# Kernel tuning notes

Measured on AMD Instinct MI355X. Metric: run time of the kernel, lower is better.

Reference implementation:

```python
import jax, jax.numpy as jnp
import numpy as np

N_NODES = 50000
N_EDGES = 800000
D_IN = 128
D_HID = 200
D_OUT = 64
EPS = 0.0  # initial_eps, train_eps=False


def setup_inputs() -> dict:
    key = jax.random.key(0)
    ks = jax.random.split(key, 8)
    x = jax.random.normal(ks[0], (N_NODES, D_IN), dtype=jnp.float32)
    edge_row = jax.random.randint(ks[1], (N_EDGES,), 0, N_NODES)
    edge_col = jax.random.randint(ks[2], (N_EDGES,), 0, N_NODES)
    edge_val = jax.random.uniform(ks[3], (N_EDGES,), dtype=jnp.float32)
    W1 = jax.random.normal(ks[4], (D_IN, D_HID), dtype=jnp.float32) * 0.05
    b1 = jnp.zeros((D_HID,), dtype=jnp.float32)
    W2 = jax.random.normal(ks[5], (D_HID, D_OUT), dtype=jnp.float32) * 0.05
    b2 = jnp.zeros((D_OUT,), dtype=jnp.float32)
    return {"x": x, "edge_row": edge_row, "edge_col": edge_col,
            "edge_val": edge_val, "W1": W1, "b1": b1, "W2": W2, "b2": b2}


def reference(x, edge_row, edge_col, edge_val, W1, b1, W2, b2):
    # SpMM: agg[i] = sum_e val[e] * x[col[e]] for edges with row[e] == i
    msgs = edge_val[:, None] * x[edge_col]            # [E, D_IN] gather
    agg = jax.ops.segment_sum(msgs, edge_row, num_segments=N_NODES)  # [N, D_IN]
    # (1 + eps) * x + A @ x, then 2-layer MLP (Linear -> ReLU -> Linear)
    h = (1.0 + EPS) * x + agg
    h = jax.nn.relu(h @ W1 + b1)                      # [N, D_HID]
    out = h @ W2 + b2                                 # [N, D_OUT]
    return out
```

## Files before the change

### kernel.cpp

```cpp
#include <hip/hip_runtime.h>

#define NN 50000
#define NE 800000
#define DIN 128
#define DH 200
#define DHP 256
#define DO 64
#define RPB 32
#define NBUCK 1564
#define CAP 1024
#define EPB 8192
#define NBLK_E ((NE + EPB - 1) / EPB)
#define CVT_B 1563
#define PACK_B 12
#define NBIN 256

typedef float f32x4 __attribute__((ext_vector_type(4)));
typedef short bf16x8 __attribute__((ext_vector_type(8)));
typedef short s16x4 __attribute__((ext_vector_type(4)));
typedef unsigned int uint;

__device__ __forceinline__ unsigned short f2bf(float f) {
  unsigned int b = __float_as_uint(f);
  b = (b + 0x7FFFu + ((b >> 16) & 1u)) >> 16;
  return (unsigned short)b;
}
__device__ __forceinline__ float bf2f(unsigned short u) {
  return __uint_as_float((unsigned int)u << 16);
}

__global__ __launch_bounds__(512) void k_prep(const float* __restrict__ x,
                                              uint* __restrict__ xb,
                                              const int* __restrict__ row,
                                              int* __restrict__ hist,
                                              const float* __restrict__ W1,
                                              const float* __restrict__ W2,
                                              unsigned short* __restrict__ B1p,
                                              unsigned short* __restrict__ B2p) {
  __shared__ int lh[NBUCK];
  const int bid = blockIdx.x;
  const int tid = threadIdx.x;
  if (bid < CVT_B) {
    int i = bid * 512 + tid;
    if (i < NE) {
      f32x4 a = *reinterpret_cast<const f32x4*>(x + (size_t)i * 8);
      f32x4 b = *reinterpret_cast<const f32x4*>(x + (size_t)i * 8 + 4);
      uint4 o;
      o.x = (uint)f2bf(a[0]) | ((uint)f2bf(a[1]) << 16);
      o.y = (uint)f2bf(a[2]) | ((uint)f2bf(a[3]) << 16);
      o.z = (uint)f2bf(b[0]) | ((uint)f2bf(b[1]) << 16);
      o.w = (uint)f2bf(b[2]) | ((uint)f2bf(b[3]) << 16);
      *reinterpret_cast<uint4*>(xb + (size_t)i * 4) = o;
    }
  } else if (bid < CVT_B + NBLK_E) {
    const int hb = bid - CVT_B;
    const int e0 = hb * EPB;
    for (int j = tid; j < NBUCK; j += 512) lh[j] = 0;
    __syncthreads();
#pragma unroll
    for (int p = 0; p < EPB / 512; ++p) {
      int e = e0 + p * 512 + tid;
      if (e < NE) atomicAdd(&lh[row[e] >> 5], 1);
    }
    __syncthreads();
    int* hrow = hist + (size_t)hb * NBUCK;
    for (int j = tid; j < NBUCK; j += 512) hrow[j] = lh[j];
  } else {
    int gidx = (bid - CVT_B - NBLK_E) * 512 + tid;
    if (gidx < 4096) {
      int idx = gidx;
      int lane = idx & 63;
      int s = (idx >> 6) & 3;
      int t = idx >> 8;
      int n = t * 16 + (lane & 15);
      unsigned short v[8];
#pragma unroll
      for (int j = 0; j < 8; ++j) {
        int k = s * 32 + (j & 3) + ((lane >> 4) << 2) + ((j >> 2) << 4);
        float f = (n < DH) ? W1[(size_t)k * DH + n] : 0.f;
        v[j] = f2bf(f);
      }
      *reinterpret_cast<uint4*>(B1p + (size_t)idx * 8) =
          *reinterpret_cast<const uint4*>(v);
    } else if (gidx < 6144) {
      int idx = gidx - 4096;
      int lane = idx & 63;
      int s = (idx >> 6) & 7;
      int t = idx >> 9;
      int n = t * 16 + (lane & 15);
      unsigned short v[8];
#pragma unroll
      for (int j = 0; j < 8; ++j) {
        int k = s * 32 + (j & 3) + ((lane >> 4) << 2) + ((j >> 2) << 4);
        float f = (k < DH) ? W2[(size_t)k * DO + n] : 0.f;
        v[j] = f2bf(f);
      }
      *reinterpret_cast<uint4*>(B2p + (size_t)idx * 8) =
          *reinterpret_cast<const uint4*>(v);
    }
  }
}

__global__ __launch_bounds__(256) void k_scan(int* __restrict__ hist,
                                              int* __restrict__ cnt) {
  int k = blockIdx.x * 256 + threadIdx.x;
  if (k >= NBUCK) return;
  int run = 0;
  int b = 0;
  for (; b + 8 <= NBLK_E; b += 8) {
    int v0 = hist[(size_t)(b + 0) * NBUCK + k];
    int v1 = hist[(size_t)(b + 1) * NBUCK + k];
    int v2 = hist[(size_t)(b + 2) * NBUCK + k];
    int v3 = hist[(size_t)(b + 3) * NBUCK + k];
    int v4 = hist[(size_t)(b + 4) * NBUCK + k];
    int v5 = hist[(size_t)(b + 5) * NBUCK + k];
    int v6 = hist[(size_t)(b + 6) * NBUCK + k];
    int v7 = hist[(size_t)(b + 7) * NBUCK + k];
    hist[(size_t)(b + 0) * NBUCK + k] = run; run += v0;
    hist[(size_t)(b + 1) * NBUCK + k] = run; run += v1;
    hist[(size_t)(b + 2) * NBUCK + k] = run; run += v2;
    hist[(size_t)(b + 3) * NBUCK + k] = run; run += v3;
    hist[(size_t)(b + 4) * NBUCK + k] = run; run += v4;
    hist[(size_t)(b + 5) * NBUCK + k] = run; run += v5;
    hist[(size_t)(b + 6) * NBUCK + k] = run; run += v6;
    hist[(size_t)(b + 7) * NBUCK + k] = run; run += v7;
  }
  for (; b < NBLK_E; ++b) {
    int v = hist[(size_t)b * NBUCK + k];
    hist[(size_t)b * NBUCK + k] = run;
    run += v;
  }
  cnt[k] = run;
}

__global__ __launch_bounds__(512) void k_scatC(const int* __restrict__ row,
                                               const int* __restrict__ col,
                                               const float* __restrict__ val,
                                               const int* __restrict__ hist,
                                               uint2* __restrict__ ep) {
  __shared__ int lh[NBUCK];
  __shared__ int lbase[NBUCK];
  const int tid = threadIdx.x;
  const int e0 = blockIdx.x * EPB;
  const int* hrow = hist + (size_t)blockIdx.x * NBUCK;
  for (int j = tid; j < NBUCK; j += 512) { lh[j] = 0; lbase[j] = hrow[j]; }
  __syncthreads();
#pragma unroll
  for (int p = 0; p < EPB / 512; ++p) {
    int e = e0 + p * 512 + tid;
    if (e < NE) {
      int r = row[e];
      int k = r >> 5;
      int rank = atomicAdd(&lh[k], 1);
      int pos = lbase[k] + rank;
      if (pos < CAP)
        ep[(size_t)k * CAP + pos] =
            make_uint2((uint)col[e] | ((uint)(r & (RPB - 1)) << 16),
                       __float_as_uint(val[e]));
    }
  }
}

__global__ __launch_bounds__(256, 8) void k_spmm_mlp(const uint* __restrict__ xbu,
                                                     const uint2* __restrict__ ep,
                                                     const int* __restrict__ cnt,
                                                     const unsigned short* __restrict__ B1p,
                                                     const float* __restrict__ b1,
                                                     const unsigned short* __restrict__ B2p,
                                                     const float* __restrict__ b2,
                                                     float* __restrict__ out) {
  __shared__ uint2 buf2[2112];
  __shared__ int deg2[NBIN], rbase2[NBIN], rpos2[NBIN];
  __shared__ int ws[4];
  uint2* se = buf2;
  unsigned short* hb = (unsigned short*)(buf2 + CAP);
  unsigned short* hs = (unsigned short*)buf2;
  const int tid = threadIdx.x;
  const int bucket = blockIdx.x;
  const int r0 = bucket * RPB;
  const int w = tid >> 6, lane = tid & 63;
  const int g = lane >> 4, r16 = lane & 15;
  const int half = lane >> 5, l32 = lane & 31;

  deg2[tid] = 0;
  __syncthreads();

  int n = cnt[bucket];
  if (n > CAP) n = CAP;
  const uint2* eb = ep + (size_t)bucket * CAP;

  uint2 rec[4];
  int key[4];
#pragma unroll
  for (int q = 0; q < 4; ++q) {
    int j = q * 256 + tid;
    rec[q] = (j < n) ? eb[j] : make_uint2(0u, 0u);
    key[q] = (int)(((rec[q].x >> 16) & (RPB - 1)) * 8 + ((rec[q].x & 0xFFFFu) >> 13));
  }
#pragma unroll
  for (int q = 0; q < 4; ++q)
    if (q * 256 + tid < n) atomicAdd(&deg2[key[q]], 1);
  __syncthreads();

  {
    int v = deg2[tid];
    int incl = v;
#pragma unroll
    for (int d = 1; d < 64; d <<= 1) {
      int t = __shfl_up(incl, d, 64);
      if (lane >= d) incl += t;
    }
    if (lane == 63) ws[w] = incl;
    __syncthreads();
    if (tid == 0) {
      int s = 0;
#pragma unroll
      for (int q = 0; q < 4; ++q) { int xx = ws[q]; ws[q] = s; s += xx; }
    }
    __syncthreads();
    int excl = ws[w] + incl - v;
    rbase2[tid] = excl;
    rpos2[tid] = excl;
  }
  __syncthreads();

#pragma unroll
  for (int q = 0; q < 4; ++q)
    if (q * 256 + tid < n) {
      int p = atomicAdd(&rpos2[key[q]], 1);
      se[p] = make_uint2(rec[q].x & 0xFFFFu, rec[q].y);
    }
  __syncthreads();

  const uint2* xb2 = reinterpret_cast<const uint2*>(xbu);
  for (int rr = w; rr < RPB; rr += 4) {
    int gr = r0 + rr;
    if (gr >= NN) {
      if (half == 0)
        *reinterpret_cast<uint2*>(&hb[rr * 136 + 4 * l32]) = make_uint2(0u, 0u);
      continue;
    }
    int s = rbase2[rr * 8];
    int en = (rr < RPB - 1) ? rbase2[(rr + 1) * 8] : n;
    float a0 = 0.f, a1 = 0.f, a2 = 0.f, a3 = 0.f;
    int j = s + half;
    for (; j + 6 < en; j += 8) {
      uint2 e0 = se[j], e1 = se[j + 2], e2 = se[j + 4], e3 = se[j + 6];
      uint2 q0 = xb2[(size_t)e0.x * 32 + l32];
      uint2 q1 = xb2[(size_t)e1.x * 32 + l32];
      uint2 q2 = xb2[(size_t)e2.x * 32 + l32];
      uint2 q3 = xb2[(size_t)e3.x * 32 + l32];
      float v0 = __uint_as_float(e0.y), v1 = __uint_as_float(e1.y);
      float v2 = __uint_as_float(e2.y), v3 = __uint_as_float(e3.y);
      a0 += v0 * bf2f((unsigned short)q0.x) + v1 * bf2f((unsigned short)q1.x) +
            v2 * bf2f((unsigned short)q2.x) + v3 * bf2f((unsigned short)q3.x);
      a1 += v0 * bf2f((unsigned short)(q0.x >> 16)) + v1 * bf2f((unsigned short)(q1.x >> 16)) +
            v2 * bf2f((unsigned short)(q2.x >> 16)) + v3 * bf2f((unsigned short)(q3.x >> 16));
      a2 += v0 * bf2f((unsigned short)q0.y) + v1 * bf2f((unsigned short)q1.y) +
            v2 * bf2f((unsigned short)q2.y) + v3 * bf2f((unsigned short)q3.y);
      a3 += v0 * bf2f((unsigned short)(q0.y >> 16)) + v1 * bf2f((unsigned short)(q1.y >> 16)) +
            v2 * bf2f((unsigned short)(q2.y >> 16)) + v3 * bf2f((unsigned short)(q3.y >> 16));
    }
    for (; j < en; j += 2) {
      uint2 e0 = se[j];
      uint2 q0 = xb2[(size_t)e0.x * 32 + l32];
      float v0 = __uint_as_float(e0.y);
      a0 += v0 * bf2f((unsigned short)q0.x);
      a1 += v0 * bf2f((unsigned short)(q0.x >> 16));
      a2 += v0 * bf2f((unsigned short)q0.y);
      a3 += v0 * bf2f((unsigned short)(q0.y >> 16));
    }
    a0 += __shfl_xor(a0, 32, 64);
    a1 += __shfl_xor(a1, 32, 64);
    a2 += __shfl_xor(a2, 32, 64);
    a3 += __shfl_xor(a3, 32, 64);
    uint2 xs = xb2[(size_t)gr * 32 + l32];
    a0 += bf2f((unsigned short)xs.x);
    a1 += bf2f((unsigned short)(xs.x >> 16));
    a2 += bf2f((unsigned short)xs.y);
    a3 += bf2f((unsigned short)(xs.y >> 16));
    if (half == 0) {
      uint2 o;
      o.x = (uint)f2bf(a0) | ((uint)f2bf(a1) << 16);
      o.y = (uint)f2bf(a2) | ((uint)f2bf(a3) << 16);
      *reinterpret_cast<uint2*>(&hb[rr * 136 + 4 * l32]) = o;
    }
  }
  __syncthreads();

  f32x4 acc[2][4];
#pragma unroll
  for (int a = 0; a < 2; ++a)
#pragma unroll
    for (int b = 0; b < 4; ++b)
#pragma unroll
      for (int c = 0; c < 4; ++c) acc[a][b][c] = 0.f;

  for (int s = 0; s < 4; ++s) {
    bf16x8 af[2];
#pragma unroll
    for (int mr = 0; mr < 2; ++mr) {
      const unsigned short* p = &hb[(mr * 16 + r16) * 136 + s * 32 + g * 4];
      s16x4 lo4 = *reinterpret_cast<const s16x4*>(p);
      s16x4 hi4 = *reinterpret_cast<const s16x4*>(p + 16);
#pragma unroll
      for (int j = 0; j < 4; ++j) { af[mr][j] = lo4[j]; af[mr][4 + j] = hi4[j]; }
    }
#pragma unroll
    for (int nr = 0; nr < 4; ++nr) {
      int t = w * 4 + nr;
      bf16x8 bf = *reinterpret_cast<const bf16x8*>(B1p + (size_t)((t * 4 + s) * 64 + lane) * 8);
      acc[0][nr] = __builtin_amdgcn_mfma_f32_16x16x32_bf16(af[0], bf, acc[0][nr], 0, 0, 0);
      acc[1][nr] = __builtin_amdgcn_mfma_f32_16x16x32_bf16(af[1], bf, acc[1][nr], 0, 0, 0);
    }
  }
  __syncthreads();
#pragma unroll
  for (int mr = 0; mr < 2; ++mr)
#pragma unroll
    for (int nr = 0; nr < 4; ++nr) {
      int nn = w * 64 + nr * 16 + r16;
      float bias = (nn < DH) ? b1[nn] : 0.f;
#pragma unroll
      for (int i = 0; i < 4; ++i) {
        int rl = mr * 16 + g * 4 + i;
        float v = acc[mr][nr][i] + bias;
        v = v > 0.f ? v : 0.f;
        if (nn >= DH) v = 0.f;
        hs[rl * 260 + nn] = f2bf(v);
      }
    }
  __syncthreads();

  f32x4 acc2[2];
#pragma unroll
  for (int b = 0; b < 2; ++b)
#pragma unroll
    for (int c = 0; c < 4; ++c) acc2[b][c] = 0.f;

  for (int s = 0; s < 8; ++s) {
#pragma unroll
    for (int mt = 0; mt < 2; ++mt) {
      const unsigned short* p = &hs[(mt * 16 + r16) * 260 + s * 32 + g * 4];
      s16x4 lo4 = *reinterpret_cast<const s16x4*>(p);
      s16x4 hi4 = *reinterpret_cast<const s16x4*>(p + 16);
      bf16x8 af;
#pragma unroll
      for (int j = 0; j < 4; ++j) { af[j] = lo4[j]; af[4 + j] = hi4[j]; }
      bf16x8 bf = *reinterpret_cast<const bf16x8*>(B2p + (size_t)((w * 8 + s) * 64 + lane) * 8);
      acc2[mt] = __builtin_amdgcn_mfma_f32_16x16x32_bf16(af, bf, acc2[mt], 0, 0, 0);
    }
  }
#pragma unroll
  for (int mt = 0; mt < 2; ++mt) {
    int nn = w * 16 + r16;
    float bias = b2[nn];
#pragma unroll
    for (int i = 0; i < 4; ++i) {
      int grow = r0 + mt * 16 + g * 4 + i;
      if (grow < NN) out[(size_t)grow * DO + nn] = acc2[mt][i] + bias;
    }
  }
}

extern "C" void kernel_launch(void* const* d_in, const int* in_sizes, int n_in,
                              void* d_out, int out_size, void* d_ws, size_t ws_size,
                              hipStream_t stream) {
  const float* x = (const float*)d_in[0];
  const int* erow = (const int*)d_in[1];
  const int* ecol = (const int*)d_in[2];
  const float* eval_ = (const float*)d_in[3];
  const float* W1 = (const float*)d_in[4];
  const float* b1 = (const float*)d_in[5];
  const float* W2 = (const float*)d_in[6];
  const float* b2 = (const float*)d_in[7];
  float* out = (float*)d_out;

  char* ws = (char*)d_ws;
  size_t o = 0;
  uint* xb = (uint*)(ws + o);          o += (size_t)NN * 64 * 4;
  unsigned short* B1p = (unsigned short*)(ws + o); o += 32768 * 2;
  unsigned short* B2p = (unsigned short*)(ws + o); o += 16384 * 2;
  o = (o + 255) & ~(size_t)255;
  int* cnt = (int*)(ws + o);           o += (NBUCK * 4 + 255) & ~(size_t)255;
  int* hist = (int*)(ws + o);          o += (size_t)NBLK_E * NBUCK * 4;
  o = (o + 255) & ~(size_t)255;
  uint2* ep = (uint2*)(ws + o);

  k_prep<<<CVT_B + NBLK_E + PACK_B, 512, 0, stream>>>(x, xb, erow, hist, W1, W2, B1p, B2p);
  k_scan<<<(NBUCK + 255) / 256, 256, 0, stream>>>(hist, cnt);
  k_scatC<<<NBLK_E, 512, 0, stream>>>(erow, ecol, eval_, hist, ep);
  k_spmm_mlp<<<NBUCK, 256, 0, stream>>>(xb, ep, cnt, B1p, b1, B2p, b2, out);
}
```

Baseline: 76.85 us.

## Move x conversion and weight packing into the scan kernel, run histogram first

The histogram now runs as its own kernel. The x-to-bf16 conversion and the weight packing move out of the first kernel and into the scan kernel, so the tiny 7-block scan runs alongside that bulk work instead of as a lone launch. This is meant to hide the scan's poor occupancy and shorten the critical path. The SpMM inner loop is also restructured so all four gathers are issued before any accumulation, and the accumulation order changes slightly, which may alter floating-point rounding.

```diff
diff --git a/kernel.cpp b/kernel.cpp
--- a/kernel.cpp
+++ b/kernel.cpp
@@ -11,8 +11,9 @@
 #define CAP 1024
 #define EPB 8192
 #define NBLK_E ((NE + EPB - 1) / EPB)
-#define CVT_B 1563
-#define PACK_B 12
+#define SCAN_B 7
+#define CVT_B 3125
+#define PACK_B 24
 #define NBIN 256
 
 typedef float f32x4 __attribute__((ext_vector_type(4)));
@@ -29,44 +30,71 @@
   return __uint_as_float((unsigned int)u << 16);
 }
 
-__global__ __launch_bounds__(512) void k_prep(const float* __restrict__ x,
-                                              uint* __restrict__ xb,
-                                              const int* __restrict__ row,
-                                              int* __restrict__ hist,
-                                              const float* __restrict__ W1,
-                                              const float* __restrict__ W2,
-                                              unsigned short* __restrict__ B1p,
-                                              unsigned short* __restrict__ B2p) {
+__global__ __launch_bounds__(512) void k_hist(const int* __restrict__ row,
+                                              int* __restrict__ hist) {
   __shared__ int lh[NBUCK];
+  const int tid = threadIdx.x;
+  const int e0 = blockIdx.x * EPB;
+  for (int j = tid; j < NBUCK; j += 512) lh[j] = 0;
+  __syncthreads();
+#pragma unroll
+  for (int p = 0; p < EPB / 512; ++p) {
+    int e = e0 + p * 512 + tid;
+    if (e < NE) atomicAdd(&lh[row[e] >> 5], 1);
+  }
+  __syncthreads();
+  int* hrow = hist + (size_t)blockIdx.x * NBUCK;
+  for (int j = tid; j < NBUCK; j += 512) hrow[j] = lh[j];
+}
+
+__global__ __launch_bounds__(256) void k_scan_cvt_pack(
+    int* __restrict__ hist, int* __restrict__ cnt,
+    const float* __restrict__ x, uint* __restrict__ xb,
+    const float* __restrict__ W1, const float* __restrict__ W2,
+    unsigned short* __restrict__ B1p, unsigned short* __restrict__ B2p) {
   const int bid = blockIdx.x;
   const int tid = threadIdx.x;
-  if (bid < CVT_B) {
-    int i = bid * 512 + tid;
-    if (i < NE) {
-      f32x4 a = *reinterpret_cast<const f32x4*>(x + (size_t)i * 8);
-      f32x4 b = *reinterpret_cast<const f32x4*>(x + (size_t)i * 8 + 4);
-      uint4 o;
-      o.x = (uint)f2bf(a[0]) | ((uint)f2bf(a[1]) << 16);
-      o.y = (uint)f2bf(a[2]) | ((uint)f2bf(a[3]) << 16);
-      o.z = (uint)f2bf(b[0]) | ((uint)f2bf(b[1]) << 16);
-      o.w = (uint)f2bf(b[2]) | ((uint)f2bf(b[3]) << 16);
-      *reinterpret_cast<uint4*>(xb + (size_t)i * 4) = o;
-    }
-  } else if (bid < CVT_B + NBLK_E) {
-    const int hb = bid - CVT_B;
-    const int e0 = hb * EPB;
-    for (int j = tid; j < NBUCK; j += 512) lh[j] = 0;
-    __syncthreads();
-#pragma unroll
-    for (int p = 0; p < EPB / 512; ++p) {
-      int e = e0 + p * 512 + tid;
-      if (e < NE) atomicAdd(&lh[row[e] >> 5], 1);
-    }
-    __syncthreads();
-    int* hrow = hist + (size_t)hb * NBUCK;
-    for (int j = tid; j < NBUCK; j += 512) hrow[j] = lh[j];
+  if (bid < SCAN_B) {
+    int k = bid * 256 + tid;
+    if (k >= NBUCK) return;
+    int run = 0;
+    int b = 0;
+    for (; b + 8 <= NBLK_E; b += 8) {
+      int v0 = hist[(size_t)(b + 0) * NBUCK + k];
+      int v1 = hist[(size_t)(b + 1) * NBUCK + k];
+      int v2 = hist[(size_t)(b + 2) * NBUCK + k];
+      int v3 = hist[(size_t)(b + 3) * NBUCK + k];
+      int v4 = hist[(size_t)(b + 4) * NBUCK + k];
+      int v5 = hist[(size_t)(b + 5) * NBUCK + k];
+      int v6 = hist[(size_t)(b + 6) * NBUCK + k];
+      int v7 = hist[(size_t)(b + 7) * NBUCK + k];
+      hist[(size_t)(b + 0) * NBUCK + k] = run; run += v0;
+      hist[(size_t)(b + 1) * NBUCK + k] = run; run += v1;
+      hist[(size_t)(b + 2) * NBUCK + k] = run; run += v2;
+      hist[(size_t)(b + 3) * NBUCK + k] = run; run += v3;
+      hist[(size_t)(b + 4) * NBUCK + k] = run; run += v4;
+      hist[(size_t)(b + 5) * NBUCK + k] = run; run += v5;
+      hist[(size_t)(b + 6) * NBUCK + k] = run; run += v6;
+      hist[(size_t)(b + 7) * NBUCK + k] = run; run += v7;
+    }
+    for (; b < NBLK_E; ++b) {
+      int v = hist[(size_t)b * NBUCK + k];
+      hist[(size_t)b * NBUCK + k] = run;
+      run += v;
+    }
+    cnt[k] = run;
+  } else if (bid < SCAN_B + CVT_B) {
+    int i = (bid - SCAN_B) * 256 + tid;
+    f32x4 a = *reinterpret_cast<const f32x4*>(x + (size_t)i * 8);
+    f32x4 b = *reinterpret_cast<const f32x4*>(x + (size_t)i * 8 + 4);
+    uint4 o;
+    o.x = (uint)f2bf(a[0]) | ((uint)f2bf(a[1]) << 16);
+    o.y = (uint)f2bf(a[2]) | ((uint)f2bf(a[3]) << 16);
+    o.z = (uint)f2bf(b[0]) | ((uint)f2bf(b[1]) << 16);
+    o.w = (uint)f2bf(b[2]) | ((uint)f2bf(b[3]) << 16);
+    *reinterpret_cast<uint4*>(xb + (size_t)i * 4) = o;
   } else {
-    int gidx = (bid - CVT_B - NBLK_E) * 512 + tid;
+    int gidx = (bid - SCAN_B - CVT_B) * 256 + tid;
     if (gidx < 4096) {
       int idx = gidx;
       int lane = idx & 63;
@@ -99,38 +127,6 @@
           *reinterpret_cast<const uint4*>(v);
     }
   }
-}
-
-__global__ __launch_bounds__(256) void k_scan(int* __restrict__ hist,
-                                              int* __restrict__ cnt) {
-  int k = blockIdx.x * 256 + threadIdx.x;
-  if (k >= NBUCK) return;
-  int run = 0;
-  int b = 0;
-  for (; b + 8 <= NBLK_E; b += 8) {
-    int v0 = hist[(size_t)(b + 0) * NBUCK + k];
-    int v1 = hist[(size_t)(b + 1) * NBUCK + k];
-    int v2 = hist[(size_t)(b + 2) * NBUCK + k];
-    int v3 = hist[(size_t)(b + 3) * NBUCK + k];
-    int v4 = hist[(size_t)(b + 4) * NBUCK + k];
-    int v5 = hist[(size_t)(b + 5) * NBUCK + k];
-    int v6 = hist[(size_t)(b + 6) * NBUCK + k];
-    int v7 = hist[(size_t)(b + 7) * NBUCK + k];
-    hist[(size_t)(b + 0) * NBUCK + k] = run; run += v0;
-    hist[(size_t)(b + 1) * NBUCK + k] = run; run += v1;
-    hist[(size_t)(b + 2) * NBUCK + k] = run; run += v2;
-    hist[(size_t)(b + 3) * NBUCK + k] = run; run += v3;
-    hist[(size_t)(b + 4) * NBUCK + k] = run; run += v4;
-    hist[(size_t)(b + 5) * NBUCK + k] = run; run += v5;
-    hist[(size_t)(b + 6) * NBUCK + k] = run; run += v6;
-    hist[(size_t)(b + 7) * NBUCK + k] = run; run += v7;
-  }
-  for (; b < NBLK_E; ++b) {
-    int v = hist[(size_t)b * NBUCK + k];
-    hist[(size_t)b * NBUCK + k] = run;
-    run += v;
-  }
-  cnt[k] = run;
 }
 
 __global__ __launch_bounds__(512) void k_scatC(const int* __restrict__ row,
@@ -245,21 +241,19 @@
     float a0 = 0.f, a1 = 0.f, a2 = 0.f, a3 = 0.f;
     int j = s + half;
     for (; j + 6 < en; j += 8) {
-      uint2 e0 = se[j], e1 = se[j + 2], e2 = se[j + 4], e3 = se[j + 6];
-      uint2 q0 = xb2[(size_t)e0.x * 32 + l32];
-      uint2 q1 = xb2[(size_t)e1.x * 32 + l32];
-      uint2 q2 = xb2[(size_t)e2.x * 32 + l32];
-      uint2 q3 = xb2[(size_t)e3.x * 32 + l32];
-      float v0 = __uint_as_float(e0.y), v1 = __uint_as_float(e1.y);
-      float v2 = __uint_as_float(e2.y), v3 = __uint_as_float(e3.y);
-      a0 += v0 * bf2f((unsigned short)q0.x) + v1 * bf2f((unsigned short)q1.x) +
-            v2 * bf2f((unsigned short)q2.x) + v3 * bf2f((unsigned short)q3.x);
-      a1 += v0 * bf2f((unsigned short)(q0.x >> 16)) + v1 * bf2f((unsigned short)(q1.x >> 16)) +
-            v2 * bf2f((unsigned short)(q2.x >> 16)) + v3 * bf2f((unsigned short)(q3.x >> 16));
-      a2 += v0 * bf2f((unsigned short)q0.y) + v1 * bf2f((unsigned short)q1.y) +
-            v2 * bf2f((unsigned short)q2.y) + v3 * bf2f((unsigned short)q3.y);
-      a3 += v0 * bf2f((unsigned short)(q0.y >> 16)) + v1 * bf2f((unsigned short)(q1.y >> 16)) +
-            v2 * bf2f((unsigned short)(q2.y >> 16)) + v3 * bf2f((unsigned short)(q3.y >> 16));
+      uint2 e[4], qv[4];
+#pragma unroll
+      for (int t = 0; t < 4; ++t) e[t] = se[j + 2 * t];
+#pragma unroll
+      for (int t = 0; t < 4; ++t) qv[t] = xb2[(size_t)e[t].x * 32 + l32];
+#pragma unroll
+      for (int t = 0; t < 4; ++t) {
+        float v = __uint_as_float(e[t].y);
+        a0 += v * bf2f((unsigned short)qv[t].x);
+        a1 += v * bf2f((unsigned short)(qv[t].x >> 16));
+        a2 += v * bf2f((unsigned short)qv[t].y);
+        a3 += v * bf2f((unsigned short)(qv[t].y >> 16));
+      }
     }
     for (; j < en; j += 2) {
       uint2 e0 = se[j];
@@ -387,8 +381,9 @@
   o = (o + 255) & ~(size_t)255;
   uint2* ep = (uint2*)(ws + o);
 
-  k_prep<<<CVT_B + NBLK_E + PACK_B, 512, 0, stream>>>(x, xb, erow, hist, W1, W2, B1p, B2p);
-  k_scan<<<(NBUCK + 255) / 256, 256, 0, stream>>>(hist, cnt);
+  k_hist<<<NBLK_E, 512, 0, stream>>>(erow, hist);
+  k_scan_cvt_pack<<<SCAN_B + CVT_B + PACK_B, 256, 0, stream>>>(
+      hist, cnt, x, xb, W1, W2, B1p, B2p);
   k_scatC<<<NBLK_E, 512, 0, stream>>>(erow, ecol, eval_, hist, ep);
   k_spmm_mlp<<<NBUCK, 256, 0, stream>>>(xb, ep, cnt, B1p, b1, B2p, b2, out);
 }
```

New measurement: 76.57 us. Within noise of the previous version (-0.4%).
